# Performance work log

Measured on AMD Instinct MI355X. Metric: run time of the kernel, lower is better.

The kernel has to match this reference:

```python
import jax, jax.numpy as jnp
import numpy as np
from jax import lax

B, T = 8192, 128
HID = 64


def setup_inputs() -> dict:
    key = jax.random.key(0)
    ks = jax.random.split(key, 16)
    actor_ids = jax.random.randint(ks[0], (B, T), 0, 7, dtype=jnp.int32)
    action_ids = jax.random.randint(ks[1], (B, T), 0, 4, dtype=jnp.int32)
    street_ids = jax.random.randint(ks[2], (B, T), 0, 5, dtype=jnp.int32)
    bet_fraction = jax.random.uniform(ks[3], (B, T, 1), dtype=jnp.float32)
    # prefix-valid mask from random lengths (some zero-length rows)
    lengths = jax.random.randint(ks[4], (B,), 0, T + 1)
    valid_mask = jnp.arange(T)[None, :] < lengths[:, None]  # [B,T] bool
    s = 0.1
    params = {
        "E_actor": jax.random.normal(ks[5], (7, 8), jnp.float32) * s,
        "E_action": jax.random.normal(ks[6], (4, 8), jnp.float32) * s,
        "E_street": jax.random.normal(ks[7], (5, 4), jnp.float32) * s,
        "W_proj": jax.random.normal(ks[8], (32, 21), jnp.float32) * s,
        "b_proj": jax.random.normal(ks[9], (32,), jnp.float32) * s,
        "W_ih": jax.random.normal(ks[10], (3 * HID, 32), jnp.float32) * s,
        "W_hh": jax.random.normal(ks[11], (3 * HID, HID), jnp.float32) * s,
        "b_ih": jax.random.normal(ks[12], (3 * HID,), jnp.float32) * s,
        "b_hh": jax.random.normal(ks[13], (3 * HID,), jnp.float32) * s,
    }
    return dict(actor_ids=actor_ids, action_ids=action_ids, street_ids=street_ids,
                bet_fraction=bet_fraction, valid_mask=valid_mask, **params)


def reference(actor_ids, action_ids, street_ids, bet_fraction, valid_mask,
              E_actor, E_action, E_street, W_proj, b_proj,
              W_ih, W_hh, b_ih, b_hh):
    # embed + concat -> [B,T,21]
    feats = jnp.concatenate([E_actor[actor_ids], E_action[action_ids],
                             E_street[street_ids], bet_fraction], axis=-1)
    x = feats @ W_proj.T + b_proj                      # [B,T,32]
    # precompute input-side GRU gates for all timesteps: [B,T,3H]
    xg = x @ W_ih.T + b_ih
    xg_t = jnp.swapaxes(xg, 0, 1)                      # [T,B,3H]
    m_t = jnp.swapaxes(valid_mask, 0, 1)               # [T,B]

    def step(h, inp):
        xg_i, m = inp
        hg = h @ W_hh.T + b_hh                         # [B,3H]
        xr, xz, xn = jnp.split(xg_i, 3, axis=-1)
        hr, hz, hn = jnp.split(hg, 3, axis=-1)
        r = jax.nn.sigmoid(xr + hr)
        z = jax.nn.sigmoid(xz + hz)
        n = jnp.tanh(xn + r * hn)
        h_new = (1.0 - z) * n + z * h
        # only advance hidden state while t < length (prefix-valid mask);
        # final carry equals the GRU hidden at the last valid step, and rows
        # with length 0 stay at the zero init (matches torch masking).
        h = jnp.where(m[:, None], h_new, h)
        return h, None

    h0 = jnp.zeros((x.shape[0], HID), dtype=x.dtype)
    h_final, _ = lax.scan(step, h0, (xg_t, m_t))
    return h_final
```

## Files before the change

kernel.cpp:

```cpp
#include <hip/hip_runtime.h>

#define HID 64
#define TT  128
#define NROWS 8192
#define NGRP (NROWS / 8)
#define LOG2E 1.44269504088896f

typedef _Float16 half8 __attribute__((ext_vector_type(8)));
typedef float    f32x4 __attribute__((ext_vector_type(4)));


__global__ void k_len(const int* __restrict__ mask, int* __restrict__ lens) {
    const int row = blockIdx.x * 4 + (threadIdx.x >> 6);
    const int l   = threadIdx.x & 63;
    const int* mrow = mask + row * TT;
    int c = (mrow[l] != 0) + (mrow[l + 64] != 0);
    #pragma unroll
    for (int k = 32; k >= 1; k >>= 1) c += __shfl_xor(c, k);
    if (l == 0) lens[row] = c;
}

__global__ __launch_bounds__(1024) void k_sort(const int* __restrict__ lens,
                                               int* __restrict__ perm) {
    __shared__ int hist[TT + 1];
    __shared__ int offs[TT + 1];
    const int tid = threadIdx.x;
    if (tid <= TT) hist[tid] = 0;
    __syncthreads();
    int myL[8];
    #pragma unroll
    for (int i = 0; i < 8; i++) {
        myL[i] = lens[tid + 1024 * i];
        atomicAdd(&hist[myL[i]], 1);
    }
    __syncthreads();
    if (tid <= TT) {
        int s = 0;
        for (int j = 0; j < tid; j++) s += hist[j];
        offs[tid] = s;
    }
    __syncthreads();
    #pragma unroll
    for (int i = 0; i < 8; i++) {
        const int pos = atomicAdd(&offs[myL[i]], 1);
        const int d   = NROWS - 1 - pos;
        const int g8  = d >> 3, r = d & 7;
        int b;
        if      (g8 < 256) b = g8;
        else if (g8 < 512) b = 256 + (511 - g8);
        else if (g8 < 768) b = 512 + (g8 - 512);
        else               b = 768 + (1023 - g8);
        perm[b * 8 + r] = tid + 1024 * i;
    }
}

__global__ __launch_bounds__(256, 4) void gru_fused(
    const int* __restrict__ actor_ids, const int* __restrict__ action_ids,
    const int* __restrict__ street_ids, const float* __restrict__ bet,
    const float* __restrict__ E_actor, const float* __restrict__ E_action,
    const float* __restrict__ E_street, const float* __restrict__ W_proj,
    const float* __restrict__ b_proj, const float* __restrict__ W_ih,
    const float* __restrict__ b_ih, const float* __restrict__ W_hh,
    const float* __restrict__ b_hh, const int* __restrict__ perm,
    const int* __restrict__ lens, float* __restrict__ out)
{
    __shared__ __align__(16) union {
        float wfs[192][32];
        struct {
            int pb[TT][9];
            __align__(16) _Float16 hb[2][8][72];
            int Lsh[8];
            int Psh[8];
        } c;
    } A;
    __shared__ __align__(16) _Float16 embl[8][136];
    __shared__ float bfs[192];

    const int tid = threadIdx.x;
    const int wv  = tid >> 6;
    const int l   = tid & 63;
    const int q   = l >> 4;
    const int cc  = l & 15;
    const int cr  = cc & 7;
    const int hf  = cc >> 3;
    const int g   = blockIdx.x;
    const int ec  = l & 7;

    for (int i = tid; i < 136; i += 256) {
        int r = i >> 3, m = i & 7;
        float v = 0.f;
        if (r < 7)       v = E_actor[r * 8 + m];
        else if (r < 11) v = E_action[(r - 7) * 8 + m];
        else if (r < 16) v = (m < 4) ? E_street[(r - 11) * 4 + m] : 0.f;
        const _Float16 hv = (_Float16)v;
        #pragma unroll
        for (int c8 = 0; c8 < 8; c8++) embl[c8][i] = hv;
    }

    if (tid < 192) {
        const int j = tid;
        float wf[21];
        #pragma unroll
        for (int m = 0; m < 21; m++) wf[m] = 0.f;
        float bf = b_ih[j];
        for (int k = 0; k < 32; k++) {
            const float w = W_ih[j * 32 + k];
            bf += w * b_proj[k];
            #pragma unroll
            for (int m = 0; m < 21; m++) wf[m] += w * W_proj[k * 21 + m];
        }
        const float s = (j < 128) ? LOG2E : 2.f * LOG2E;
        #pragma unroll
        for (int m = 0; m < 21; m++) A.wfs[j][m] = wf[m] * s;
        #pragma unroll
        for (int m = 21; m < 32; m++) A.wfs[j][m] = 0.f;
        bfs[j] = bf;
    }
    __syncthreads();

    half8 Af[3], Ah[3][2];
    {
        const int m16 = l & 15, kq = l >> 4;
        #pragma unroll
        for (int g3 = 0; g3 < 3; g3++) {
            const int jr = g3 * 64 + wv * 16 + m16;
            _Float16 v[8];
            #pragma unroll
            for (int m = 0; m < 8; m++) v[m] = (_Float16)A.wfs[jr][kq * 8 + m];
            Af[g3] = *(half8*)v;
            const float s = (g3 < 2) ? LOG2E : 2.f * LOG2E;
            #pragma unroll
            for (int kt = 0; kt < 2; kt++) {
                _Float16 w[8];
                #pragma unroll
                for (int m = 0; m < 8; m++)
                    w[m] = (_Float16)(W_hh[jr * HID + kt * 32 + kq * 8 + m] * s);
                Ah[g3][kt] = *(half8*)w;
            }
        }
    }
    f32x4 biasR, biasZ, biasX, biasH;
    #pragma unroll
    for (int e = 0; e < 4; e++) {
        const int idx = 16 * wv + 4 * q + e;
        biasR[e] = (bfs[idx]      + b_hh[idx])      * LOG2E;
        biasZ[e] = (bfs[64 + idx] + b_hh[64 + idx]) * LOG2E;
        biasX[e] = bfs[128 + idx]  * (2.f * LOG2E);
        biasH[e] = b_hh[128 + idx] * (2.f * LOG2E);
    }
    __syncthreads();

    for (int i = tid; i < 2 * 8 * 72 / 2; i += 256) ((int*)A.c.hb)[i] = 0;
    {
        const int r = tid >> 5, tl = tid & 31;
        const int prow = perm[g * 8 + r];
        const int base = prow * TT;
        #pragma unroll
        for (int i = 0; i < 4; i++) {
            const int t = tl + 32 * i;
            const int a = actor_ids[base + t], c = action_ids[base + t];
            const int s = street_ids[base + t];
            const _Float16 f16 = (_Float16)bet[base + t];
            const unsigned fb = (unsigned)*(const unsigned short*)&f16;
            A.c.pb[t][r] = (int)(a | (c << 3) | (s << 5) | (fb << 16));
        }
        if (tl == 0) { A.c.Lsh[r] = lens[prow]; A.c.Psh[r] = prow; }
    }
    __syncthreads();

    const int Ln = A.c.Lsh[cr];
    int Lmax = Ln;
    { int o = __shfl_xor(Lmax, 1); Lmax = o > Lmax ? o : Lmax; }
    { int o = __shfl_xor(Lmax, 2); Lmax = o > Lmax ? o : Lmax; }
    { int o = __shfl_xor(Lmax, 4); Lmax = o > Lmax ? o : Lmax; }

    const bool isq2 = (q == 2);
    const int sh = (q == 1) ? 3 : (q == 2) ? 5 : 0;
    const int mk = (q == 1) ? 3 : (q == 3) ? 0 : 7;
    const int of = (q == 1) ? 7 : (q == 2) ? 11 : (q == 3) ? 16 : 0;

    const int j0 = 16 * wv + 4 * q + 2 * hf;
    float h0 = 0.f, h1 = 0.f;
    const f32x4 zero4 = {0.f, 0.f, 0.f, 0.f};

    half8 BfA, BfB;
    {
        const int p0 = A.c.pb[0][cr];
        BfA = *(const half8*)&embl[ec][(((p0 >> sh) & mk) + of) * 8];
        uint4* b0 = (uint4*)&BfA;
        b0->z = isq2 ? ((unsigned)p0 >> 16) : b0->z;
        const int p1 = A.c.pb[1][cr];
        BfB = *(const half8*)&embl[ec][(((p1 >> sh) & mk) + of) * 8];
        uint4* b1 = (uint4*)&BfB;
        b1->z = isq2 ? ((unsigned)p1 >> 16) : b1->z;
    }
    f32x4 xR0 = __builtin_amdgcn_mfma_f32_16x16x32_f16(Af[0], BfA, biasR, 0, 0, 0);
    f32x4 xZ0 = __builtin_amdgcn_mfma_f32_16x16x32_f16(Af[1], BfA, biasZ, 0, 0, 0);
    f32x4 xX0 = __builtin_amdgcn_mfma_f32_16x16x32_f16(Af[2], BfA, biasX, 0, 0, 0);
    f32x4 xR1, xZ1, xX1;

    #define ACT_WRITE(aR_, aZ_, aH_, aX_, LIVE_, WB_)                              \
    {                                                                              \
        const float vR0 = hf ? aR_[2] : aR_[0], vR1 = hf ? aR_[3] : aR_[1];        \
        const float vZ0 = hf ? aZ_[2] : aZ_[0], vZ1 = hf ? aZ_[3] : aZ_[1];        \
        const float vH0 = hf ? aH_[2] : aH_[0], vH1 = hf ? aH_[3] : aH_[1];        \
        const float vX0 = hf ? aX_[2] : aX_[0], vX1 = hf ? aX_[3] : aX_[1];        \
        const float r0 = __builtin_amdgcn_rcpf(1.f + __builtin_amdgcn_exp2f(-vR0));\
        const float z0 = __builtin_amdgcn_rcpf(1.f + __builtin_amdgcn_exp2f(-vZ0));\
        const float y0 = vX0 + r0 * vH0;                                           \
        const float n0 = 1.f - 2.f * __builtin_amdgcn_rcpf(1.f + __builtin_amdgcn_exp2f(y0)); \
        const float hv0 = n0 + z0 * (h0 - n0);                                     \
        h0 = (LIVE_) ? hv0 : h0;                                                   \
        const float r1 = __builtin_amdgcn_rcpf(1.f + __builtin_amdgcn_exp2f(-vR1));\
        const float z1 = __builtin_amdgcn_rcpf(1.f + __builtin_amdgcn_exp2f(-vZ1));\
        const float y1 = vX1 + r1 * vH1;                                           \
        const float n1 = 1.f - 2.f * __builtin_amdgcn_rcpf(1.f + __builtin_amdgcn_exp2f(y1)); \
        const float hv1 = n1 + z1 * (h1 - n1);                                     \
        h1 = (LIVE_) ? hv1 : h1;                                                   \
        const _Float16 a16 = (_Float16)h0, b16 = (_Float16)h1;                     \
        const unsigned pk = (unsigned)*(const unsigned short*)&a16 |               \
                            ((unsigned)*(const unsigned short*)&b16 << 16);        \
        *(unsigned*)&A.c.hb[WB_][cr][j0] = pk;                                     \
    }

    for (int t = 0; t < Lmax; t += 2) {
        {
            const half8 Bh0 = *(const half8*)&A.c.hb[0][cr][q * 8];
            const half8 Bh1 = *(const half8*)&A.c.hb[0][cr][32 + q * 8];
            const int t2 = (t + 2 < TT) ? t + 2 : TT - 1;
            const int p2 = A.c.pb[t2][cr];

            f32x4 aRa = __builtin_amdgcn_mfma_f32_16x16x32_f16(Ah[0][0], Bh0, xR0, 0, 0, 0);
            f32x4 aRb = __builtin_amdgcn_mfma_f32_16x16x32_f16(Ah[0][1], Bh1, zero4, 0, 0, 0);
            f32x4 aZ = __builtin_amdgcn_mfma_f32_16x16x32_f16(Ah[1][0], Bh0, xZ0, 0, 0, 0);
            aZ = __builtin_amdgcn_mfma_f32_16x16x32_f16(Ah[1][1], Bh1, aZ, 0, 0, 0);
            f32x4 aH = __builtin_amdgcn_mfma_f32_16x16x32_f16(Ah[2][0], Bh0, biasH, 0, 0, 0);
            aH = __builtin_amdgcn_mfma_f32_16x16x32_f16(Ah[2][1], Bh1, aH, 0, 0, 0);
            const f32x4 aR = aRa + aRb;

            xR1 = __builtin_amdgcn_mfma_f32_16x16x32_f16(Af[0], BfB, biasR, 0, 0, 0);
            xZ1 = __builtin_amdgcn_mfma_f32_16x16x32_f16(Af[1], BfB, biasZ, 0, 0, 0);
            xX1 = __builtin_amdgcn_mfma_f32_16x16x32_f16(Af[2], BfB, biasX, 0, 0, 0);

            BfA = *(const half8*)&embl[ec][(((p2 >> sh) & mk) + of) * 8];
            uint4* bq = (uint4*)&BfA;
            bq->z = isq2 ? ((unsigned)p2 >> 16) : bq->z;

            ACT_WRITE(aR, aZ, aH, xX0, t < Ln, 1);
        }
        __syncthreads();
        {
            const half8 Bh0 = *(const half8*)&A.c.hb[1][cr][q * 8];
            const half8 Bh1 = *(const half8*)&A.c.hb[1][cr][32 + q * 8];
            const int t3 = (t + 3 < TT) ? t + 3 : TT - 1;
            const int p3 = A.c.pb[t3][cr];

            f32x4 aRa = __builtin_amdgcn_mfma_f32_16x16x32_f16(Ah[0][0], Bh0, xR1, 0, 0, 0);
            f32x4 aRb = __builtin_amdgcn_mfma_f32_16x16x32_f16(Ah[0][1], Bh1, zero4, 0, 0, 0);
            f32x4 aZ = __builtin_amdgcn_mfma_f32_16x16x32_f16(Ah[1][0], Bh0, xZ1, 0, 0, 0);
            aZ = __builtin_amdgcn_mfma_f32_16x16x32_f16(Ah[1][1], Bh1, aZ, 0, 0, 0);
            f32x4 aH = __builtin_amdgcn_mfma_f32_16x16x32_f16(Ah[2][0], Bh0, biasH, 0, 0, 0);
            aH = __builtin_amdgcn_mfma_f32_16x16x32_f16(Ah[2][1], Bh1, aH, 0, 0, 0);
            const f32x4 aR = aRa + aRb;

            xR0 = __builtin_amdgcn_mfma_f32_16x16x32_f16(Af[0], BfA, biasR, 0, 0, 0);
            xZ0 = __builtin_amdgcn_mfma_f32_16x16x32_f16(Af[1], BfA, biasZ, 0, 0, 0);
            xX0 = __builtin_amdgcn_mfma_f32_16x16x32_f16(Af[2], BfA, biasX, 0, 0, 0);

            BfB = *(const half8*)&embl[ec][(((p3 >> sh) & mk) + of) * 8];
            uint4* bq = (uint4*)&BfB;
            bq->z = isq2 ? ((unsigned)p3 >> 16) : bq->z;

            ACT_WRITE(aR, aZ, aH, xX1, t + 1 < Ln, 0);
        }
        __syncthreads();
    }
    #undef ACT_WRITE

    const int prow = A.c.Psh[cr];
    *(float2*)&out[prow * HID + j0] = make_float2(h0, h1);
}

extern "C" void kernel_launch(void* const* d_in, const int* in_sizes, int n_in,
                              void* d_out, int out_size, void* d_ws, size_t ws_size,
                              hipStream_t stream) {
    const int*   actor_ids  = (const int*)d_in[0];
    const int*   action_ids = (const int*)d_in[1];
    const int*   street_ids = (const int*)d_in[2];
    const float* bet        = (const float*)d_in[3];
    const int*   vmask      = (const int*)d_in[4];
    const float* E_actor    = (const float*)d_in[5];
    const float* E_action   = (const float*)d_in[6];
    const float* E_street   = (const float*)d_in[7];
    const float* W_proj     = (const float*)d_in[8];
    const float* b_proj     = (const float*)d_in[9];
    const float* W_ih       = (const float*)d_in[10];
    const float* W_hh       = (const float*)d_in[11];
    const float* b_ih       = (const float*)d_in[12];
    const float* b_hh       = (const float*)d_in[13];
    float*       out        = (float*)d_out;

    int* ws   = (int*)d_ws;
    int* lens = ws;
    int* perm = ws + NROWS;

    k_len<<<NROWS / 4, 256, 0, stream>>>(vmask, lens);
    k_sort<<<1, 1024, 0, stream>>>(lens, perm);

    gru_fused<<<NGRP, 256, 0, stream>>>(actor_ids, action_ids, street_ids, bet,
                                        E_actor, E_action, E_street,
                                        W_proj, b_proj, W_ih, b_ih, W_hh, b_hh,
                                        perm, lens, out);
}
```

Before: 158.8 us.

## Process two interleaved row groups per block to hide GRU step latency

```diff
diff --git a/kernel.cpp b/kernel.cpp
--- a/kernel.cpp
+++ b/kernel.cpp
@@ -3,7 +3,7 @@
 #define HID 64
 #define TT  128
 #define NROWS 8192
-#define NGRP (NROWS / 8)
+#define NGRP 512
 #define LOG2E 1.44269504088896f
 
 typedef _Float16 half8 __attribute__((ext_vector_type(8)));
@@ -45,16 +45,11 @@
         const int pos = atomicAdd(&offs[myL[i]], 1);
         const int d   = NROWS - 1 - pos;
         const int g8  = d >> 3, r = d & 7;
-        int b;
-        if      (g8 < 256) b = g8;
-        else if (g8 < 512) b = 256 + (511 - g8);
-        else if (g8 < 768) b = 512 + (g8 - 512);
-        else               b = 768 + (1023 - g8);
-        perm[b * 8 + r] = tid + 1024 * i;
-    }
-}
-
-__global__ __launch_bounds__(256, 4) void gru_fused(
+        perm[((g8 >> 1) * 2 + (g8 & 1)) * 8 + r] = tid + 1024 * i;
+    }
+}
+
+__global__ __launch_bounds__(256, 2) void gru_fused(
     const int* __restrict__ actor_ids, const int* __restrict__ action_ids,
     const int* __restrict__ street_ids, const float* __restrict__ bet,
     const float* __restrict__ E_actor, const float* __restrict__ E_action,
@@ -67,10 +62,10 @@
     __shared__ __align__(16) union {
         float wfs[192][32];
         struct {
-            int pb[TT][9];
-            __align__(16) _Float16 hb[2][8][72];
-            int Lsh[8];
-            int Psh[8];
+            int pb[2][TT][9];
+            __align__(16) _Float16 hb[2][2][8][72];
+            int Lsh[2][8];
+            int Psh[2][8];
         } c;
     } A;
     __shared__ __align__(16) _Float16 embl[8][136];
@@ -150,26 +145,29 @@
     }
     __syncthreads();
 
-    for (int i = tid; i < 2 * 8 * 72 / 2; i += 256) ((int*)A.c.hb)[i] = 0;
+    for (int i = tid; i < 2 * 2 * 8 * 72 / 2; i += 256) ((int*)A.c.hb)[i] = 0;
     {
-        const int r = tid >> 5, tl = tid & 31;
-        const int prow = perm[g * 8 + r];
+        const int r16 = tid >> 4, tl = tid & 15;
+        const int gi = r16 >> 3, r = r16 & 7;
+        const int prow = perm[(g * 2 + gi) * 8 + r];
         const int base = prow * TT;
         #pragma unroll
-        for (int i = 0; i < 4; i++) {
-            const int t = tl + 32 * i;
+        for (int i = 0; i < 8; i++) {
+            const int t = tl + 16 * i;
             const int a = actor_ids[base + t], c = action_ids[base + t];
             const int s = street_ids[base + t];
             const _Float16 f16 = (_Float16)bet[base + t];
             const unsigned fb = (unsigned)*(const unsigned short*)&f16;
-            A.c.pb[t][r] = (int)(a | (c << 3) | (s << 5) | (fb << 16));
+            A.c.pb[gi][t][r] = (int)(a | (c << 3) | (s << 5) | (fb << 16));
         }
-        if (tl == 0) { A.c.Lsh[r] = lens[prow]; A.c.Psh[r] = prow; }
-    }
-    __syncthreads();
-
-    const int Ln = A.c.Lsh[cr];
-    int Lmax = Ln;
+        if (tl == 0) { A.c.Lsh[gi][r] = lens[prow]; A.c.Psh[gi][r] = prow; }
+    }
+    __syncthreads();
+
+    int Ln[2];
+    Ln[0] = A.c.Lsh[0][cr];
+    Ln[1] = A.c.Lsh[1][cr];
+    int Lmax = Ln[0] > Ln[1] ? Ln[0] : Ln[1];
     { int o = __shfl_xor(Lmax, 1); Lmax = o > Lmax ? o : Lmax; }
     { int o = __shfl_xor(Lmax, 2); Lmax = o > Lmax ? o : Lmax; }
     { int o = __shfl_xor(Lmax, 4); Lmax = o > Lmax ? o : Lmax; }
@@ -180,105 +178,84 @@
     const int of = (q == 1) ? 7 : (q == 2) ? 11 : (q == 3) ? 16 : 0;
 
     const int j0 = 16 * wv + 4 * q + 2 * hf;
-    float h0 = 0.f, h1 = 0.f;
+    float h0[2] = {0.f, 0.f}, h1[2] = {0.f, 0.f};
     const f32x4 zero4 = {0.f, 0.f, 0.f, 0.f};
 
-    half8 BfA, BfB;
-    {
-        const int p0 = A.c.pb[0][cr];
-        BfA = *(const half8*)&embl[ec][(((p0 >> sh) & mk) + of) * 8];
-        uint4* b0 = (uint4*)&BfA;
+    half8 BfA[2], BfB[2];
+    f32x4 xR0[2], xZ0[2], xX0[2], xR1[2], xZ1[2], xX1[2];
+    #pragma unroll
+    for (int gi = 0; gi < 2; gi++) {
+        const int p0 = A.c.pb[gi][0][cr];
+        BfA[gi] = *(const half8*)&embl[ec][(((p0 >> sh) & mk) + of) * 8];
+        uint4* b0 = (uint4*)&BfA[gi];
         b0->z = isq2 ? ((unsigned)p0 >> 16) : b0->z;
-        const int p1 = A.c.pb[1][cr];
-        BfB = *(const half8*)&embl[ec][(((p1 >> sh) & mk) + of) * 8];
-        uint4* b1 = (uint4*)&BfB;
+        const int p1 = A.c.pb[gi][1][cr];
+        BfB[gi] = *(const half8*)&embl[ec][(((p1 >> sh) & mk) + of) * 8];
+        uint4* b1 = (uint4*)&BfB[gi];
         b1->z = isq2 ? ((unsigned)p1 >> 16) : b1->z;
-    }
-    f32x4 xR0 = __builtin_amdgcn_mfma_f32_16x16x32_f16(Af[0], BfA, biasR, 0, 0, 0);
-    f32x4 xZ0 = __builtin_amdgcn_mfma_f32_16x16x32_f16(Af[1], BfA, biasZ, 0, 0, 0);
-    f32x4 xX0 = __builtin_amdgcn_mfma_f32_16x16x32_f16(Af[2], BfA, biasX, 0, 0, 0);
-    f32x4 xR1, xZ1, xX1;
-
-    #define ACT_WRITE(aR_, aZ_, aH_, aX_, LIVE_, WB_)                              \
+        xR0[gi] = __builtin_amdgcn_mfma_f32_16x16x32_f16(Af[0], BfA[gi], biasR, 0, 0, 0);
+        xZ0[gi] = __builtin_amdgcn_mfma_f32_16x16x32_f16(Af[1], BfA[gi], biasZ, 0, 0, 0);
+        xX0[gi] = __builtin_amdgcn_mfma_f32_16x16x32_f16(Af[2], BfA[gi], biasX, 0, 0, 0);
+    }
+
+    #define STEP_G(gi_, RB_, WB_, xR_, xZ_, xX_, xRn_, xZn_, xXn_, BfC_, BfN_, TOFF_) \
     {                                                                              \
-        const float vR0 = hf ? aR_[2] : aR_[0], vR1 = hf ? aR_[3] : aR_[1];        \
-        const float vZ0 = hf ? aZ_[2] : aZ_[0], vZ1 = hf ? aZ_[3] : aZ_[1];        \
-        const float vH0 = hf ? aH_[2] : aH_[0], vH1 = hf ? aH_[3] : aH_[1];        \
-        const float vX0 = hf ? aX_[2] : aX_[0], vX1 = hf ? aX_[3] : aX_[1];        \
+        const half8 Bh0 = *(const half8*)&A.c.hb[gi_][RB_][cr][q * 8];             \
+        const half8 Bh1 = *(const half8*)&A.c.hb[gi_][RB_][cr][32 + q * 8];        \
+        const int tn = (t + (TOFF_) < TT) ? t + (TOFF_) : TT - 1;                  \
+        const int pn = A.c.pb[gi_][tn][cr];                                        \
+        f32x4 aRa = __builtin_amdgcn_mfma_f32_16x16x32_f16(Ah[0][0], Bh0, xR_[gi_], 0, 0, 0); \
+        f32x4 aRb = __builtin_amdgcn_mfma_f32_16x16x32_f16(Ah[0][1], Bh1, zero4, 0, 0, 0);    \
+        f32x4 aZ = __builtin_amdgcn_mfma_f32_16x16x32_f16(Ah[1][0], Bh0, xZ_[gi_], 0, 0, 0);  \
+        aZ = __builtin_amdgcn_mfma_f32_16x16x32_f16(Ah[1][1], Bh1, aZ, 0, 0, 0);   \
+        f32x4 aH = __builtin_amdgcn_mfma_f32_16x16x32_f16(Ah[2][0], Bh0, biasH, 0, 0, 0);     \
+        aH = __builtin_amdgcn_mfma_f32_16x16x32_f16(Ah[2][1], Bh1, aH, 0, 0, 0);   \
+        const f32x4 aR = aRa + aRb;                                                \
+        xRn_[gi_] = __builtin_amdgcn_mfma_f32_16x16x32_f16(Af[0], BfN_[gi_], biasR, 0, 0, 0); \
+        xZn_[gi_] = __builtin_amdgcn_mfma_f32_16x16x32_f16(Af[1], BfN_[gi_], biasZ, 0, 0, 0); \
+        xXn_[gi_] = __builtin_amdgcn_mfma_f32_16x16x32_f16(Af[2], BfN_[gi_], biasX, 0, 0, 0); \
+        BfC_[gi_] = *(const half8*)&embl[ec][(((pn >> sh) & mk) + of) * 8];        \
+        uint4* bq = (uint4*)&BfC_[gi_];                                            \
+        bq->z = isq2 ? ((unsigned)pn >> 16) : bq->z;                               \
+        const f32x4 aX = xX_[gi_];                                                 \
+        const float vR0 = hf ? aR[2] : aR[0], vR1 = hf ? aR[3] : aR[1];            \
+        const float vZ0 = hf ? aZ[2] : aZ[0], vZ1 = hf ? aZ[3] : aZ[1];            \
+        const float vH0 = hf ? aH[2] : aH[0], vH1 = hf ? aH[3] : aH[1];            \
+        const float vX0 = hf ? aX[2] : aX[0], vX1 = hf ? aX[3] : aX[1];            \
+        const bool live = (t + ((TOFF_) - 2) < Ln[gi_]);                           \
         const float r0 = __builtin_amdgcn_rcpf(1.f + __builtin_amdgcn_exp2f(-vR0));\
         const float z0 = __builtin_amdgcn_rcpf(1.f + __builtin_amdgcn_exp2f(-vZ0));\
         const float y0 = vX0 + r0 * vH0;                                           \
         const float n0 = 1.f - 2.f * __builtin_amdgcn_rcpf(1.f + __builtin_amdgcn_exp2f(y0)); \
-        const float hv0 = n0 + z0 * (h0 - n0);                                     \
-        h0 = (LIVE_) ? hv0 : h0;                                                   \
+        const float hv0 = n0 + z0 * (h0[gi_] - n0);                                \
+        h0[gi_] = live ? hv0 : h0[gi_];                                            \
         const float r1 = __builtin_amdgcn_rcpf(1.f + __builtin_amdgcn_exp2f(-vR1));\
         const float z1 = __builtin_amdgcn_rcpf(1.f + __builtin_amdgcn_exp2f(-vZ1));\
         const float y1 = vX1 + r1 * vH1;                                           \
         const float n1 = 1.f - 2.f * __builtin_amdgcn_rcpf(1.f + __builtin_amdgcn_exp2f(y1)); \
-        const float hv1 = n1 + z1 * (h1 - n1);                                     \
-        h1 = (LIVE_) ? hv1 : h1;                                                   \
-        const _Float16 a16 = (_Float16)h0, b16 = (_Float16)h1;                     \
+        const float hv1 = n1 + z1 * (h1[gi_] - n1);                                \
+        h1[gi_] = live ? hv1 : h1[gi_];                                            \
+        const _Float16 a16 = (_Float16)h0[gi_], b16 = (_Float16)h1[gi_];           \
         const unsigned pk = (unsigned)*(const unsigned short*)&a16 |               \
                             ((unsigned)*(const unsigned short*)&b16 << 16);        \
-        *(unsigned*)&A.c.hb[WB_][cr][j0] = pk;                                     \
+        *(unsigned*)&A.c.hb[gi_][WB_][cr][j0] = pk;                                \
     }
 
     for (int t = 0; t < Lmax; t += 2) {
-        {
-            const half8 Bh0 = *(const half8*)&A.c.hb[0][cr][q * 8];
-            const half8 Bh1 = *(const half8*)&A.c.hb[0][cr][32 + q * 8];
-            const int t2 = (t + 2 < TT) ? t + 2 : TT - 1;
-            const int p2 = A.c.pb[t2][cr];
-
-            f32x4 aRa = __builtin_amdgcn_mfma_f32_16x16x32_f16(Ah[0][0], Bh0, xR0, 0, 0, 0);
-            f32x4 aRb = __builtin_amdgcn_mfma_f32_16x16x32_f16(Ah[0][1], Bh1, zero4, 0, 0, 0);
-            f32x4 aZ = __builtin_amdgcn_mfma_f32_16x16x32_f16(Ah[1][0], Bh0, xZ0, 0, 0, 0);
-            aZ = __builtin_amdgcn_mfma_f32_16x16x32_f16(Ah[1][1], Bh1, aZ, 0, 0, 0);
-            f32x4 aH = __builtin_amdgcn_mfma_f32_16x16x32_f16(Ah[2][0], Bh0, biasH, 0, 0, 0);
-            aH = __builtin_amdgcn_mfma_f32_16x16x32_f16(Ah[2][1], Bh1, aH, 0, 0, 0);
-            const f32x4 aR = aRa + aRb;
-
-            xR1 = __builtin_amdgcn_mfma_f32_16x16x32_f16(Af[0], BfB, biasR, 0, 0, 0);
-            xZ1 = __builtin_amdgcn_mfma_f32_16x16x32_f16(Af[1], BfB, biasZ, 0, 0, 0);
-            xX1 = __builtin_amdgcn_mfma_f32_16x16x32_f16(Af[2], BfB, biasX, 0, 0, 0);
-
-            BfA = *(const half8*)&embl[ec][(((p2 >> sh) & mk) + of) * 8];
-            uint4* bq = (uint4*)&BfA;
-            bq->z = isq2 ? ((unsigned)p2 >> 16) : bq->z;
-
-            ACT_WRITE(aR, aZ, aH, xX0, t < Ln, 1);
-        }
+        STEP_G(0, 0, 1, xR0, xZ0, xX0, xR1, xZ1, xX1, BfA, BfB, 2);
+        STEP_G(1, 0, 1, xR0, xZ0, xX0, xR1, xZ1, xX1, BfA, BfB, 2);
         __syncthreads();
-        {
-            const half8 Bh0 = *(const half8*)&A.c.hb[1][cr][q * 8];
-            const half8 Bh1 = *(const half8*)&A.c.hb[1][cr][32 + q * 8];
-            const int t3 = (t + 3 < TT) ? t + 3 : TT - 1;
-            const int p3 = A.c.pb[t3][cr];
-
-            f32x4 aRa = __builtin_amdgcn_mfma_f32_16x16x32_f16(Ah[0][0], Bh0, xR1, 0, 0, 0);
-            f32x4 aRb = __builtin_amdgcn_mfma_f32_16x16x32_f16(Ah[0][1], Bh1, zero4, 0, 0, 0);
-            f32x4 aZ = __builtin_amdgcn_mfma_f32_16x16x32_f16(Ah[1][0], Bh0, xZ1, 0, 0, 0);
-            aZ = __builtin_amdgcn_mfma_f32_16x16x32_f16(Ah[1][1], Bh1, aZ, 0, 0, 0);
-            f32x4 aH = __builtin_amdgcn_mfma_f32_16x16x32_f16(Ah[2][0], Bh0, biasH, 0, 0, 0);
-            aH = __builtin_amdgcn_mfma_f32_16x16x32_f16(Ah[2][1], Bh1, aH, 0, 0, 0);
-            const f32x4 aR = aRa + aRb;
-
-            xR0 = __builtin_amdgcn_mfma_f32_16x16x32_f16(Af[0], BfA, biasR, 0, 0, 0);
-            xZ0 = __builtin_amdgcn_mfma_f32_16x16x32_f16(Af[1], BfA, biasZ, 0, 0, 0);
-            xX0 = __builtin_amdgcn_mfma_f32_16x16x32_f16(Af[2], BfA, biasX, 0, 0, 0);
-
-            BfB = *(const half8*)&embl[ec][(((p3 >> sh) & mk) + of) * 8];
-            uint4* bq = (uint4*)&BfB;
-            bq->z = isq2 ? ((unsigned)p3 >> 16) : bq->z;
-
-            ACT_WRITE(aR, aZ, aH, xX1, t + 1 < Ln, 0);
-        }
+        STEP_G(0, 1, 0, xR1, xZ1, xX1, xR0, xZ0, xX0, BfB, BfA, 3);
+        STEP_G(1, 1, 0, xR1, xZ1, xX1, xR0, xZ0, xX0, BfB, BfA, 3);
         __syncthreads();
     }
-    #undef ACT_WRITE
-
-    const int prow = A.c.Psh[cr];
-    *(float2*)&out[prow * HID + j0] = make_float2(h0, h1);
+    #undef STEP_G
+
+    #pragma unroll
+    for (int gi = 0; gi < 2; gi++) {
+        const int prow = A.c.Psh[gi][cr];
+        *(float2*)&out[prow * HID + j0] = make_float2(h0[gi], h1[gi]);
+    }
 }
 
 extern "C" void kernel_launch(void* const* d_in, const int* in_sizes, int n_in,
```

Result: slower. 185.9 us (+17.1%).
